# Kernel tuning notes

Hardware: AMD Instinct MI355X
Metric: run time of the kernel (lower is better)

## Reference

```python
import jax, jax.numpy as jnp
import numpy as np

B, T_MEL, T_TXT = 16, 2048, 1024
D_MODEL, D_ENC_M, D_ENC_T = 512, 512, 512
LN_EPS = 1e-5


def setup_inputs() -> dict:
    key = jax.random.key(0)
    ks = jax.random.split(key, 9)
    mel_encoding = jax.random.normal(ks[0], (B, T_MEL, D_ENC_M), dtype=jnp.float32)
    text_encoding = jax.random.normal(ks[1], (B, T_TXT, D_ENC_T), dtype=jnp.float32)
    mel_mask = jax.random.randint(ks[2], (B, T_MEL), 0, 2).astype(bool)
    mel_mask = mel_mask.at[:, 0].set(False)  # guarantee >=1 unmasked key per row
    src_mask = jax.random.randint(ks[3], (B, T_TXT), 0, 2).astype(bool)
    # Projection weights stored [in, out] (torch Linear does x @ W.T)
    sc = 1.0 / np.sqrt(D_ENC_M)
    Wq = jax.random.uniform(ks[4], (D_ENC_T, D_MODEL), jnp.float32, -sc, sc)
    Wk = jax.random.uniform(ks[5], (D_ENC_M, D_MODEL), jnp.float32, -sc, sc)
    Wv = jax.random.uniform(ks[6], (D_ENC_M, D_MODEL), jnp.float32, -sc, sc)
    ln_gamma = jnp.ones((D_MODEL,), jnp.float32)
    ln_beta = jnp.zeros((D_MODEL,), jnp.float32)
    return {"mel_encoding": mel_encoding, "text_encoding": text_encoding,
            "mel_mask": mel_mask, "src_mask": src_mask,
            "Wq": Wq, "Wk": Wk, "Wv": Wv,
            "ln_gamma": ln_gamma, "ln_beta": ln_beta}


def reference(mel_encoding, text_encoding, mel_mask, src_mask, Wq, Wk, Wv, ln_gamma, ln_beta):
    temperature = jnp.sqrt(jnp.float32(D_ENC_M))
    q = jnp.einsum('btd,dm->btm', text_encoding, Wq)   # [B, T_txt, d_model]
    k = jnp.einsum('bsd,dm->bsm', mel_encoding, Wk)    # [B, T_mel, d_model]
    v = jnp.einsum('bsd,dm->bsm', mel_encoding, Wv)
    # attn_mask = outer product of src_mask and mel_mask (True -> masked)
    attn_mask = src_mask[:, :, None] & mel_mask[:, None, :]  # [B, T_txt, T_mel]
    scores = jnp.einsum('btm,bsm->bts', q, k) / temperature
    scores = jnp.where(attn_mask, -jnp.inf, scores)
    attn = jax.nn.softmax(scores, axis=2)
    output = jnp.einsum('bts,bsm->btm', attn, v)
    # dropout is identity at inference; LayerNorm over last dim
    mean = jnp.mean(output, axis=-1, keepdims=True)
    var = jnp.var(output, axis=-1, keepdims=True)
    output = (output - mean) * jax.lax.rsqrt(var + LN_EPS) * ln_gamma + ln_beta
    return output, attn
```

## Files before the change

kernel.cpp:

```cpp
#include <hip/hip_runtime.h>

#define DEV __device__ __forceinline__

typedef __attribute__((ext_vector_type(8))) short short8v;
typedef __attribute__((ext_vector_type(4))) float f32x4;

DEV unsigned short f2bf(float f) {
  unsigned int x = __float_as_uint(f);
  x = x + 0x7FFFu + ((x >> 16) & 1u);
  return (unsigned short)(x >> 16);
}

DEV int swz_byte(int row, int kElem) {
  int chunk = ((kElem >> 3) ^ (row & 7));
  return row * 128 + (chunk << 4) + ((kElem & 7) << 1);
}

template <int ROUNDS>
DEV void stage(const unsigned short* __restrict__ g, int ld,
               unsigned short* tile, int tid) {
  const int wave = tid >> 6, l = tid & 63;
#pragma unroll
  for (int p = 0; p < ROUNDS; ++p) {
    const int r = (p << 5) + (wave << 3) + (l >> 3);
    const int c = ((l & 7) ^ (r & 7)) << 3;
    const unsigned short* src = g + (long)r * ld + c;
#if __has_builtin(__builtin_amdgcn_global_load_lds)
    unsigned short* dst = tile + (p << 11) + (wave << 9);
    __builtin_amdgcn_global_load_lds(
        (const __attribute__((address_space(1))) void*)src,
        (__attribute__((address_space(3))) void*)dst, 16, 0, 0);
#else
    short8v v = *reinterpret_cast<const short8v*>(src);
    *reinterpret_cast<short8v*>(reinterpret_cast<char*>(tile) +
                                (p << 12) + (wave << 10) + (l << 4)) = v;
#endif
  }
}

template <int BM, int EPI>
__global__ __launch_bounds__(256) void gemm_bf16(
    const unsigned short* __restrict__ A, const unsigned short* __restrict__ B,
    void* __restrict__ Cout, int M, int N, int K,
    long aBatch, long bBatch, long cBatch,
    const int* __restrict__ srcMask, const int* __restrict__ melMask,
    float scale, float* __restrict__ stats) {
  constexpr int NI = BM / 32;
  __shared__ unsigned short As[BM * 64];
  __shared__ unsigned short Bs[128 * 64];
  const int tid = threadIdx.x;
  const int lane = tid & 63;
  const int wave = tid >> 6;
  const int z = blockIdx.z;
  const unsigned short* Ab = A + (long)z * aBatch;
  const unsigned short* Bb = B + (long)z * bBatch;
  const long cOff = (long)z * cBatch;
  const int bm = blockIdx.y * BM;
  const int bn = blockIdx.x * 128;
  const int wr = (wave >> 1) * (BM / 2);
  const int wc = (wave & 1) * 64;
  const int l15 = lane & 15;
  const int lHi = lane >> 4;

  f32x4 acc[NI][4] = {};

  for (int kt = 0; kt < K; kt += 64) {
    stage<BM / 32>(Ab + (long)bm * K + kt, K, As, tid);
    stage<4>(Bb + (long)bn * K + kt, K, Bs, tid);
    __syncthreads();
#pragma unroll
    for (int ks = 0; ks < 2; ++ks) {
      const int k0 = (ks << 5) + (lHi << 3);
      short8v af[NI], bfr[4];
#pragma unroll
      for (int i = 0; i < NI; ++i)
        af[i] = *reinterpret_cast<const short8v*>(
            reinterpret_cast<const char*>(As) + swz_byte(wr + i * 16 + l15, k0));
#pragma unroll
      for (int j = 0; j < 4; ++j)
        bfr[j] = *reinterpret_cast<const short8v*>(
            reinterpret_cast<const char*>(Bs) + swz_byte(wc + j * 16 + l15, k0));
#pragma unroll
      for (int i = 0; i < NI; ++i)
#pragma unroll
        for (int j = 0; j < 4; ++j)
          acc[i][j] = __builtin_amdgcn_mfma_f32_16x16x32_bf16(af[i], bfr[j], acc[i][j], 0, 0, 0);
    }
    __syncthreads();
  }

  if constexpr (EPI >= 2) {
    __shared__ float redM[128][2];
    __shared__ float redS[128][2];
    const int wcIdx = wave & 1;
#pragma unroll
    for (int i = 0; i < NI; ++i) {
#pragma unroll
      for (int rr = 0; rr < 4; ++rr) {
        const int rloc = wr + i * 16 + lHi * 4 + rr;
        const int rb = bm + rloc;
        const bool sm = srcMask[z * 1024 + rb] != 0;
        float vals[4];
        float m_l = -3.0e38f;
#pragma unroll
        for (int j = 0; j < 4; ++j) {
          const int c = bn + wc + j * 16 + l15;
          const bool mm = melMask[z * 2048 + c] != 0;
          const float vf = (sm && mm) ? -1e30f : acc[i][j][rr] * scale;
          vals[j] = vf;
          if constexpr (EPI == 2)
            reinterpret_cast<unsigned short*>(Cout)[cOff + (long)rb * N + c] = f2bf(vf);
          else
            reinterpret_cast<float*>(Cout)[cOff + (long)rb * N + c] = vf;
          m_l = fmaxf(m_l, vf);
        }
        if (stats) {
#pragma unroll
          for (int o = 1; o < 16; o <<= 1) m_l = fmaxf(m_l, __shfl_xor(m_l, o, 64));
          float s_l = 0.f;
#pragma unroll
          for (int j = 0; j < 4; ++j) s_l += __expf(vals[j] - m_l);
#pragma unroll
          for (int o = 1; o < 16; o <<= 1) s_l += __shfl_xor(s_l, o, 64);
          if (l15 == 0) { redM[rloc][wcIdx] = m_l; redS[rloc][wcIdx] = s_l; }
        }
      }
    }
    if (stats) {
      __syncthreads();
      if (tid < 128) {
        const float m0 = redM[tid][0], m1 = redM[tid][1];
        const float Mx = fmaxf(m0, m1);
        const float S = redS[tid][0] * __expf(m0 - Mx) + redS[tid][1] * __expf(m1 - Mx);
        const long sidx = ((long)(z * 1024 + bm + tid)) * 32 + (long)blockIdx.x * 2;
        stats[sidx] = Mx;
        stats[sidx + 1] = S;
      }
    }
  } else {
#pragma unroll
    for (int i = 0; i < NI; ++i) {
#pragma unroll
      for (int j = 0; j < 4; ++j) {
        const int rb = bm + wr + i * 16 + lHi * 4;
        const int c = bn + wc + j * 16 + l15;
#pragma unroll
        for (int r = 0; r < 4; ++r) {
          const float v = acc[i][j][r];
          const long idx = cOff + (long)(rb + r) * N + c;
          if constexpr (EPI == 0)
            reinterpret_cast<unsigned short*>(Cout)[idx] = f2bf(v);
          else
            reinterpret_cast<float*>(Cout)[idx] = v;
        }
      }
    }
  }
}

__global__ __launch_bounds__(256) void softmax_finalize(
    unsigned short* __restrict__ sbf, const float* __restrict__ stats,
    float* __restrict__ attn) {
  const long row = blockIdx.x;
  const float* st = stats + row * 32;
  float Mx = -3.0e38f;
#pragma unroll
  for (int t = 0; t < 16; ++t) Mx = fmaxf(Mx, st[t * 2]);
  float S = 0.f;
#pragma unroll
  for (int t = 0; t < 16; ++t) S += st[t * 2 + 1] * __expf(st[t * 2] - Mx);
  const float inv = 1.0f / S;
  const int tid = threadIdx.x;
  unsigned short* sp = sbf + row * 2048 + tid * 8;
  float* ap = attn + row * 2048 + tid * 8;
  const short8v sv = *reinterpret_cast<const short8v*>(sp);
  float e[8];
#pragma unroll
  for (int u = 0; u < 8; ++u) {
    const float s = __uint_as_float(((unsigned)(unsigned short)sv[u]) << 16);
    e[u] = __expf(s - Mx) * inv;
  }
  float4 w0, w1;
  w0.x = e[0]; w0.y = e[1]; w0.z = e[2]; w0.w = e[3];
  w1.x = e[4]; w1.y = e[5]; w1.z = e[6]; w1.w = e[7];
  *reinterpret_cast<float4*>(ap) = w0;
  *reinterpret_cast<float4*>(ap + 4) = w1;
  short8v pk;
#pragma unroll
  for (int u = 0; u < 8; ++u) pk[u] = (short)f2bf(e[u]);
  *reinterpret_cast<short8v*>(sp) = pk;
}

__global__ __launch_bounds__(256) void softmax_rows(
    float* __restrict__ attn, unsigned short* __restrict__ pbf) {
  const long row = blockIdx.x;
  float4* p = reinterpret_cast<float4*>(attn + row * 2048);
  const int tid = threadIdx.x;
  float4 a = p[tid];
  float4 b = p[tid + 256];
  float m = fmaxf(fmaxf(fmaxf(a.x, a.y), fmaxf(a.z, a.w)),
                  fmaxf(fmaxf(b.x, b.y), fmaxf(b.z, b.w)));
#pragma unroll
  for (int o = 32; o; o >>= 1) m = fmaxf(m, __shfl_xor(m, o, 64));
  __shared__ float redm[4];
  if ((tid & 63) == 0) redm[tid >> 6] = m;
  __syncthreads();
  m = fmaxf(fmaxf(redm[0], redm[1]), fmaxf(redm[2], redm[3]));
  float e0 = __expf(a.x - m), e1 = __expf(a.y - m), e2 = __expf(a.z - m), e3 = __expf(a.w - m);
  float e4 = __expf(b.x - m), e5 = __expf(b.y - m), e6 = __expf(b.z - m), e7 = __expf(b.w - m);
  float s = ((e0 + e1) + (e2 + e3)) + ((e4 + e5) + (e6 + e7));
#pragma unroll
  for (int o = 32; o; o >>= 1) s += __shfl_xor(s, o, 64);
  __shared__ float reds[4];
  if ((tid & 63) == 0) reds[tid >> 6] = s;
  __syncthreads();
  s = (reds[0] + reds[1]) + (reds[2] + reds[3]);
  const float inv = 1.0f / s;
  a.x = e0 * inv; a.y = e1 * inv; a.z = e2 * inv; a.w = e3 * inv;
  b.x = e4 * inv; b.y = e5 * inv; b.z = e6 * inv; b.w = e7 * inv;
  p[tid] = a;
  p[tid + 256] = b;
  ushort4 o0, o1;
  o0.x = f2bf(a.x); o0.y = f2bf(a.y); o0.z = f2bf(a.z); o0.w = f2bf(a.w);
  o1.x = f2bf(b.x); o1.y = f2bf(b.y); o1.z = f2bf(b.z); o1.w = f2bf(b.w);
  *reinterpret_cast<ushort4*>(pbf + row * 2048 + tid * 4) = o0;
  *reinterpret_cast<ushort4*>(pbf + row * 2048 + 1024 + tid * 4) = o1;
}

__global__ __launch_bounds__(256) void f32_to_bf16(
    const float* __restrict__ in, unsigned short* __restrict__ out, long n) {
  long i = ((long)blockIdx.x * blockDim.x + threadIdx.x) * 8;
  const long stride = (long)gridDim.x * blockDim.x * 8;
  for (; i < n; i += stride) {
    const float4 a = *reinterpret_cast<const float4*>(in + i);
    const float4 b = *reinterpret_cast<const float4*>(in + i + 4);
    short8v o;
    o[0] = (short)f2bf(a.x); o[1] = (short)f2bf(a.y);
    o[2] = (short)f2bf(a.z); o[3] = (short)f2bf(a.w);
    o[4] = (short)f2bf(b.x); o[5] = (short)f2bf(b.y);
    o[6] = (short)f2bf(b.z); o[7] = (short)f2bf(b.w);
    *reinterpret_cast<short8v*>(out + i) = o;
  }
}

__global__ __launch_bounds__(256) void transpose_w3(
    const float* __restrict__ Wq, const float* __restrict__ Wk, const float* __restrict__ Wv,
    unsigned short* __restrict__ WqT, unsigned short* __restrict__ WkT,
    unsigned short* __restrict__ WvT) {
  __shared__ float t[32][33];
  const int zz = blockIdx.z;
  const float* W = zz == 0 ? Wq : zz == 1 ? Wk : Wv;
  unsigned short* WT = zz == 0 ? WqT : zz == 1 ? WkT : WvT;
  const int bx = blockIdx.x * 32;
  const int by = blockIdx.y * 32;
  const int tx = threadIdx.x, ty = threadIdx.y;
#pragma unroll
  for (int i = 0; i < 4; ++i)
    t[ty + i * 8][tx] = W[(long)(by + ty + i * 8) * 512 + bx + tx];
  __syncthreads();
#pragma unroll
  for (int i = 0; i < 4; ++i)
    WT[(long)(bx + ty + i * 8) * 512 + by + tx] = f2bf(t[tx][ty + i * 8]);
}

__global__ __launch_bounds__(64) void layernorm_rows(
    float* __restrict__ out, const float* __restrict__ gamma, const float* __restrict__ beta) {
  const long row = blockIdx.x;
  float4* p = reinterpret_cast<float4*>(out + row * 512);
  const int lane = threadIdx.x;
  float4 a = p[lane];
  float4 b = p[lane + 64];
  float s = ((a.x + a.y) + (a.z + a.w)) + ((b.x + b.y) + (b.z + b.w));
  float s2 = ((a.x * a.x + a.y * a.y) + (a.z * a.z + a.w * a.w)) +
             ((b.x * b.x + b.y * b.y) + (b.z * b.z + b.w * b.w));
#pragma unroll
  for (int o = 32; o; o >>= 1) {
    s += __shfl_xor(s, o, 64);
    s2 += __shfl_xor(s2, o, 64);
  }
  const float mean = s * (1.0f / 512.0f);
  const float var = s2 * (1.0f / 512.0f) - mean * mean;
  const float rstd = rsqrtf(var + 1e-5f);
  const float4 g0 = reinterpret_cast<const float4*>(gamma)[lane];
  const float4 g1 = reinterpret_cast<const float4*>(gamma)[lane + 64];
  const float4 c0 = reinterpret_cast<const float4*>(beta)[lane];
  const float4 c1 = reinterpret_cast<const float4*>(beta)[lane + 64];
  a.x = (a.x - mean) * rstd * g0.x + c0.x;
  a.y = (a.y - mean) * rstd * g0.y + c0.y;
  a.z = (a.z - mean) * rstd * g0.z + c0.z;
  a.w = (a.w - mean) * rstd * g0.w + c0.w;
  b.x = (b.x - mean) * rstd * g1.x + c1.x;
  b.y = (b.y - mean) * rstd * g1.y + c1.y;
  b.z = (b.z - mean) * rstd * g1.z + c1.z;
  b.w = (b.w - mean) * rstd * g1.w + c1.w;
  p[lane] = a;
  p[lane + 64] = b;
}

extern "C" void kernel_launch(void* const* d_in, const int* in_sizes, int n_in,
                              void* d_out, int out_size, void* d_ws, size_t ws_size,
                              hipStream_t stream) {
  const float* mel  = (const float*)d_in[0];
  const float* text = (const float*)d_in[1];
  const int* melMask = (const int*)d_in[2];
  const int* srcMask = (const int*)d_in[3];
  const float* Wq = (const float*)d_in[4];
  const float* Wk = (const float*)d_in[5];
  const float* Wv = (const float*)d_in[6];
  const float* gamma = (const float*)d_in[7];
  const float* beta  = (const float*)d_in[8];

  float* out = (float*)d_out;
  float* attn = (float*)d_out + (long)16 * 1024 * 512;

  unsigned short* ws = (unsigned short*)d_ws;
  unsigned short* wqT = ws;
  unsigned short* wkT = wqT + 512 * 512;
  unsigned short* wvT = wkT + 512 * 512;
  unsigned short* melbf  = wvT + 512 * 512;
  unsigned short* textbf = melbf + (long)16 * 2048 * 512;
  unsigned short* qbf = textbf + (long)16 * 1024 * 512;
  unsigned short* kbf = qbf + (long)16 * 1024 * 512;
  unsigned short* vT  = kbf + (long)16 * 2048 * 512;
  unsigned short* sbf = vT + (long)16 * 512 * 2048;
  float* stats = (float*)melbf;
  const bool bigws = ws_size >= 202899456ull;

  transpose_w3<<<dim3(16, 16, 3), dim3(32, 8), 0, stream>>>(Wq, Wk, Wv, wqT, wkT, wvT);
  f32_to_bf16<<<dim3(4096), 256, 0, stream>>>(mel, melbf, (long)16 * 2048 * 512);
  f32_to_bf16<<<dim3(2048), 256, 0, stream>>>(text, textbf, (long)16 * 1024 * 512);

  gemm_bf16<128, 0><<<dim3(4, 128, 1), 256, 0, stream>>>(
      textbf, wqT, qbf, 16384, 512, 512, 0, 0, 0, nullptr, nullptr, 1.0f, nullptr);
  gemm_bf16<128, 0><<<dim3(4, 256, 1), 256, 0, stream>>>(
      melbf, wkT, kbf, 32768, 512, 512, 0, 0, 0, nullptr, nullptr, 1.0f, nullptr);
  gemm_bf16<128, 0><<<dim3(16, 4, 16), 256, 0, stream>>>(
      wvT, melbf, vT, 512, 2048, 512, 0, (long)2048 * 512, (long)512 * 2048,
      nullptr, nullptr, 1.0f, nullptr);

  if (bigws) {
    gemm_bf16<128, 2><<<dim3(16, 8, 16), 256, 0, stream>>>(
        qbf, kbf, sbf, 1024, 2048, 512,
        (long)1024 * 512, (long)2048 * 512, (long)1024 * 2048,
        srcMask, melMask, 0.044194173824159216f, stats);
    softmax_finalize<<<dim3(16 * 1024), 256, 0, stream>>>(sbf, stats, attn);
    gemm_bf16<64, 1><<<dim3(4, 16, 16), 256, 0, stream>>>(
        sbf, vT, out, 1024, 512, 2048,
        (long)1024 * 2048, (long)512 * 2048, (long)1024 * 512,
        nullptr, nullptr, 1.0f, nullptr);
  } else {
    unsigned short* pbf = melbf;
    gemm_bf16<128, 3><<<dim3(16, 8, 16), 256, 0, stream>>>(
        qbf, kbf, attn, 1024, 2048, 512,
        (long)1024 * 512, (long)2048 * 512, (long)1024 * 2048,
        srcMask, melMask, 0.044194173824159216f, nullptr);
    softmax_rows<<<dim3(16 * 1024), 256, 0, stream>>>(attn, pbf);
    gemm_bf16<64, 1><<<dim3(4, 16, 16), 256, 0, stream>>>(
        pbf, vT, out, 1024, 512, 2048,
        (long)1024 * 2048, (long)512 * 2048, (long)1024 * 512,
        nullptr, nullptr, 1.0f, nullptr);
  }
  layernorm_rows<<<dim3(16 * 1024), 64, 0, stream>>>(out, gamma, beta);
}
```

Baseline: 312.7 us.

## Fuse K/V projections and softmax normalization into PV GEMM with XCD-aware block mapping

Merges the separate K and V projection GEMMs into one kernel that stages each mel tile once and computes both outputs. The softmax finalize pass is folded into the PV GEMM: it rebuilds the row max and sum from per-tile stats, normalizes scores on the fly while loading the A tile, and writes fp32 attn from only the first N-tile. Block indices are remapped so consecutive batches land on the same XCD group, aiming for better L2 reuse. The cost is extra exp work in the PV kernel, more LDS use in gemm_kv, and irregular attn writes from a subset of blocks.

Result: no change. 310.7 us (-0.7%).

```diff
diff --git a/kernel.cpp b/kernel.cpp
--- a/kernel.cpp
+++ b/kernel.cpp
@@ -9,6 +9,9 @@
   unsigned int x = __float_as_uint(f);
   x = x + 0x7FFFu + ((x >> 16) & 1u);
   return (unsigned short)(x >> 16);
+}
+DEV float bf2f(unsigned short u) {
+  return __uint_as_float(((unsigned)u) << 16);
 }
 
 DEV int swz_byte(int row, int kElem) {
@@ -38,7 +41,7 @@
   }
 }
 
-template <int BM, int EPI>
+template <int BM, int EPI, int GM>
 __global__ __launch_bounds__(256) void gemm_bf16(
     const unsigned short* __restrict__ A, const unsigned short* __restrict__ B,
     void* __restrict__ Cout, int M, int N, int K,
@@ -51,12 +54,23 @@
   const int tid = threadIdx.x;
   const int lane = tid & 63;
   const int wave = tid >> 6;
-  const int z = blockIdx.z;
+  int z, bmi, bni;
+  if constexpr (GM == 1) {
+    const int id = blockIdx.x;
+    z = (id & 7) | ((id >> 10) << 3);
+    const int ib = (id >> 3) & 127;
+    bni = ib & 15;
+    bmi = ib >> 4;
+  } else if constexpr (GM == 2) {
+    bmi = blockIdx.x; bni = blockIdx.y; z = blockIdx.z;
+  } else {
+    bni = blockIdx.x; bmi = blockIdx.y; z = blockIdx.z;
+  }
+  const int bm = bmi * BM;
+  const int bn = bni * 128;
   const unsigned short* Ab = A + (long)z * aBatch;
   const unsigned short* Bb = B + (long)z * bBatch;
   const long cOff = (long)z * cBatch;
-  const int bm = blockIdx.y * BM;
-  const int bn = blockIdx.x * 128;
   const int wr = (wave >> 1) * (BM / 2);
   const int wc = (wave & 1) * 64;
   const int l15 = lane & 15;
@@ -132,7 +146,7 @@
         const float m0 = redM[tid][0], m1 = redM[tid][1];
         const float Mx = fmaxf(m0, m1);
         const float S = redS[tid][0] * __expf(m0 - Mx) + redS[tid][1] * __expf(m1 - Mx);
-        const long sidx = ((long)(z * 1024 + bm + tid)) * 32 + (long)blockIdx.x * 2;
+        const long sidx = ((long)(z * 1024 + bm + tid)) * 32 + (long)bni * 2;
         stats[sidx] = Mx;
         stats[sidx + 1] = S;
       }
@@ -158,37 +172,176 @@
   }
 }
 
-__global__ __launch_bounds__(256) void softmax_finalize(
-    unsigned short* __restrict__ sbf, const float* __restrict__ stats,
-    float* __restrict__ attn) {
-  const long row = blockIdx.x;
-  const float* st = stats + row * 32;
-  float Mx = -3.0e38f;
-#pragma unroll
-  for (int t = 0; t < 16; ++t) Mx = fmaxf(Mx, st[t * 2]);
-  float S = 0.f;
-#pragma unroll
-  for (int t = 0; t < 16; ++t) S += st[t * 2 + 1] * __expf(st[t * 2] - Mx);
-  const float inv = 1.0f / S;
-  const int tid = threadIdx.x;
-  unsigned short* sp = sbf + row * 2048 + tid * 8;
-  float* ap = attn + row * 2048 + tid * 8;
-  const short8v sv = *reinterpret_cast<const short8v*>(sp);
-  float e[8];
-#pragma unroll
-  for (int u = 0; u < 8; ++u) {
-    const float s = __uint_as_float(((unsigned)(unsigned short)sv[u]) << 16);
-    e[u] = __expf(s - Mx) * inv;
-  }
-  float4 w0, w1;
-  w0.x = e[0]; w0.y = e[1]; w0.z = e[2]; w0.w = e[3];
-  w1.x = e[4]; w1.y = e[5]; w1.z = e[6]; w1.w = e[7];
-  *reinterpret_cast<float4*>(ap) = w0;
-  *reinterpret_cast<float4*>(ap + 4) = w1;
-  short8v pk;
-#pragma unroll
-  for (int u = 0; u < 8; ++u) pk[u] = (short)f2bf(e[u]);
-  *reinterpret_cast<short8v*>(sp) = pk;
+__global__ __launch_bounds__(256) void gemm_kv(
+    const unsigned short* __restrict__ mel, const unsigned short* __restrict__ WkT,
+    const unsigned short* __restrict__ WvT, unsigned short* __restrict__ kbf,
+    unsigned short* __restrict__ vT) {
+  __shared__ unsigned short Ms[128 * 64];
+  __shared__ unsigned short Ks[128 * 64];
+  __shared__ unsigned short Vs[128 * 64];
+  const int id = blockIdx.x;
+  const int z = (id & 7) | ((id >> 9) << 3);
+  const int ib = (id >> 3) & 63;
+  const int st = ib & 15, mt = ib >> 4;
+  const int bs = st * 128, bmm = mt * 128;
+  const int tid = threadIdx.x, lane = tid & 63, wave = tid >> 6;
+  const int wrS = (wave >> 1) * 64, wcM = (wave & 1) * 64;
+  const int l15 = lane & 15, lHi = lane >> 4;
+  const unsigned short* melB = mel + ((long)z * 2048 + bs) * 512;
+
+  f32x4 ak[4][4] = {};
+  f32x4 av[4][4] = {};
+
+  for (int kt = 0; kt < 512; kt += 64) {
+    stage<4>(melB + kt, 512, Ms, tid);
+    stage<4>(WkT + (long)bmm * 512 + kt, 512, Ks, tid);
+    stage<4>(WvT + (long)bmm * 512 + kt, 512, Vs, tid);
+    __syncthreads();
+#pragma unroll
+    for (int ks = 0; ks < 2; ++ks) {
+      const int k0 = (ks << 5) + (lHi << 3);
+      short8v mf[4], wf[4];
+#pragma unroll
+      for (int i = 0; i < 4; ++i)
+        mf[i] = *reinterpret_cast<const short8v*>(
+            reinterpret_cast<const char*>(Ms) + swz_byte(wrS + i * 16 + l15, k0));
+#pragma unroll
+      for (int j = 0; j < 4; ++j)
+        wf[j] = *reinterpret_cast<const short8v*>(
+            reinterpret_cast<const char*>(Ks) + swz_byte(wcM + j * 16 + l15, k0));
+#pragma unroll
+      for (int i = 0; i < 4; ++i)
+#pragma unroll
+        for (int j = 0; j < 4; ++j)
+          ak[i][j] = __builtin_amdgcn_mfma_f32_16x16x32_bf16(mf[i], wf[j], ak[i][j], 0, 0, 0);
+#pragma unroll
+      for (int j = 0; j < 4; ++j)
+        wf[j] = *reinterpret_cast<const short8v*>(
+            reinterpret_cast<const char*>(Vs) + swz_byte(wcM + j * 16 + l15, k0));
+#pragma unroll
+      for (int i = 0; i < 4; ++i)
+#pragma unroll
+        for (int j = 0; j < 4; ++j)
+          av[j][i] = __builtin_amdgcn_mfma_f32_16x16x32_bf16(wf[j], mf[i], av[j][i], 0, 0, 0);
+    }
+    __syncthreads();
+  }
+
+#pragma unroll
+  for (int i = 0; i < 4; ++i)
+#pragma unroll
+    for (int j = 0; j < 4; ++j) {
+      const int srow = bs + wrS + i * 16 + lHi * 4;
+      const int mcol = bmm + wcM + j * 16 + l15;
+      const int mrow = bmm + wcM + j * 16 + lHi * 4;
+      const int scol = bs + wrS + i * 16 + l15;
+#pragma unroll
+      for (int rr = 0; rr < 4; ++rr) {
+        kbf[((long)z * 2048 + srow + rr) * 512 + mcol] = f2bf(ak[i][j][rr]);
+        vT[((long)z * 512 + mrow + rr) * 2048 + scol] = f2bf(av[j][i][rr]);
+      }
+    }
+}
+
+__global__ __launch_bounds__(256) void pv_smx(
+    const unsigned short* __restrict__ sbf, const unsigned short* __restrict__ vT,
+    float* __restrict__ attn, float* __restrict__ out,
+    const float* __restrict__ stats) {
+  __shared__ unsigned short As[64 * 64];
+  __shared__ unsigned short Bs[128 * 64];
+  __shared__ float rowM[64], rowInv[64];
+  const int id = blockIdx.x;
+  const int z = (id & 7) | ((id >> 9) << 3);
+  const int ib = (id >> 3) & 63;
+  const int mt = ib & 15, nt = ib >> 4;
+  const int bm = mt * 64, bn = nt * 128;
+  const int tid = threadIdx.x, lane = tid & 63, wave = tid >> 6;
+  const bool writeAttn = (nt == 0);
+
+  if (tid < 64) {
+    const float* st = stats + ((long)(z * 1024 + bm + tid)) * 32;
+    float Mx = -3.0e38f;
+#pragma unroll
+    for (int t = 0; t < 16; ++t) Mx = fmaxf(Mx, st[t * 2]);
+    float S = 0.f;
+#pragma unroll
+    for (int t = 0; t < 16; ++t) S += st[t * 2 + 1] * __expf(st[t * 2] - Mx);
+    rowM[tid] = Mx;
+    rowInv[tid] = 1.0f / S;
+  }
+  __syncthreads();
+
+  const int ar = tid >> 2;
+  const int ac = (tid & 3) << 4;
+  const float mR = rowM[ar];
+  const float invR = rowInv[ar];
+  const long aOff = ((long)z * 1024 + bm + ar) * 2048 + ac;
+  const unsigned short* vTb = vT + ((long)z * 512 + bn) * 2048;
+  const int wr = (wave >> 1) * 32, wc = (wave & 1) * 64;
+  const int l15 = lane & 15, lHi = lane >> 4;
+
+  f32x4 acc[2][4] = {};
+
+  for (int kt = 0; kt < 2048; kt += 64) {
+    stage<4>(vTb + kt, 2048, Bs, tid);
+    const short8v s0 = *reinterpret_cast<const short8v*>(sbf + aOff + kt);
+    const short8v s1 = *reinterpret_cast<const short8v*>(sbf + aOff + kt + 8);
+    float e[16];
+#pragma unroll
+    for (int u = 0; u < 8; ++u) {
+      e[u] = __expf(bf2f((unsigned short)s0[u]) - mR) * invR;
+      e[u + 8] = __expf(bf2f((unsigned short)s1[u]) - mR) * invR;
+    }
+    if (writeAttn) {
+      float* ap = attn + aOff + kt;
+#pragma unroll
+      for (int g = 0; g < 4; ++g) {
+        float4 w;
+        w.x = e[g * 4]; w.y = e[g * 4 + 1]; w.z = e[g * 4 + 2]; w.w = e[g * 4 + 3];
+        *reinterpret_cast<float4*>(ap + g * 4) = w;
+      }
+    }
+    short8v pk0, pk1;
+#pragma unroll
+    for (int u = 0; u < 8; ++u) {
+      pk0[u] = (short)f2bf(e[u]);
+      pk1[u] = (short)f2bf(e[u + 8]);
+    }
+    *reinterpret_cast<short8v*>(reinterpret_cast<char*>(As) + swz_byte(ar, ac)) = pk0;
+    *reinterpret_cast<short8v*>(reinterpret_cast<char*>(As) + swz_byte(ar, ac + 8)) = pk1;
+    __syncthreads();
+
+#pragma unroll
+    for (int ks = 0; ks < 2; ++ks) {
+      const int k0 = (ks << 5) + (lHi << 3);
+      short8v af[2], bfr[4];
+#pragma unroll
+      for (int i = 0; i < 2; ++i)
+        af[i] = *reinterpret_cast<const short8v*>(
+            reinterpret_cast<const char*>(As) + swz_byte(wr + i * 16 + l15, k0));
+#pragma unroll
+      for (int j = 0; j < 4; ++j)
+        bfr[j] = *reinterpret_cast<const short8v*>(
+            reinterpret_cast<const char*>(Bs) + swz_byte(wc + j * 16 + l15, k0));
+#pragma unroll
+      for (int i = 0; i < 2; ++i)
+#pragma unroll
+        for (int j = 0; j < 4; ++j)
+          acc[i][j] = __builtin_amdgcn_mfma_f32_16x16x32_bf16(af[i], bfr[j], acc[i][j], 0, 0, 0);
+    }
+    __syncthreads();
+  }
+
+#pragma unroll
+  for (int i = 0; i < 2; ++i)
+#pragma unroll
+    for (int j = 0; j < 4; ++j) {
+      const int row = bm + wr + i * 16 + lHi * 4;
+      const int col = bn + wc + j * 16 + l15;
+#pragma unroll
+      for (int rr = 0; rr < 4; ++rr)
+        out[((long)z * 1024 + row + rr) * 512 + col] = acc[i][j][rr];
+    }
 }
 
 __global__ __launch_bounds__(256) void softmax_rows(
@@ -330,32 +483,24 @@
   f32_to_bf16<<<dim3(4096), 256, 0, stream>>>(mel, melbf, (long)16 * 2048 * 512);
   f32_to_bf16<<<dim3(2048), 256, 0, stream>>>(text, textbf, (long)16 * 1024 * 512);
 
-  gemm_bf16<128, 0><<<dim3(4, 128, 1), 256, 0, stream>>>(
+  gemm_bf16<128, 0, 2><<<dim3(128, 4, 1), 256, 0, stream>>>(
       textbf, wqT, qbf, 16384, 512, 512, 0, 0, 0, nullptr, nullptr, 1.0f, nullptr);
-  gemm_bf16<128, 0><<<dim3(4, 256, 1), 256, 0, stream>>>(
-      melbf, wkT, kbf, 32768, 512, 512, 0, 0, 0, nullptr, nullptr, 1.0f, nullptr);
-  gemm_bf16<128, 0><<<dim3(16, 4, 16), 256, 0, stream>>>(
-      wvT, melbf, vT, 512, 2048, 512, 0, (long)2048 * 512, (long)512 * 2048,
-      nullptr, nullptr, 1.0f, nullptr);
+  gemm_kv<<<dim3(1024), 256, 0, stream>>>(melbf, wkT, wvT, kbf, vT);
 
   if (bigws) {
-    gemm_bf16<128, 2><<<dim3(16, 8, 16), 256, 0, stream>>>(
+    gemm_bf16<128, 2, 1><<<dim3(2048), 256, 0, stream>>>(
         qbf, kbf, sbf, 1024, 2048, 512,
         (long)1024 * 512, (long)2048 * 512, (long)1024 * 2048,
         srcMask, melMask, 0.044194173824159216f, stats);
-    softmax_finalize<<<dim3(16 * 1024), 256, 0, stream>>>(sbf, stats, attn);
-    gemm_bf16<64, 1><<<dim3(4, 16, 16), 256, 0, stream>>>(
-        sbf, vT, out, 1024, 512, 2048,
-        (long)1024 * 2048, (long)512 * 2048, (long)1024 * 512,
-        nullptr, nullptr, 1.0f, nullptr);
+    pv_smx<<<dim3(1024), 256, 0, stream>>>(sbf, vT, attn, out, stats);
   } else {
     unsigned short* pbf = melbf;
-    gemm_bf16<128, 3><<<dim3(16, 8, 16), 256, 0, stream>>>(
+    gemm_bf16<128, 3, 0><<<dim3(16, 8, 16), 256, 0, stream>>>(
         qbf, kbf, attn, 1024, 2048, 512,
         (long)1024 * 512, (long)2048 * 512, (long)1024 * 2048,
         srcMask, melMask, 0.044194173824159216f, nullptr);
     softmax_rows<<<dim3(16 * 1024), 256, 0, stream>>>(attn, pbf);
-    gemm_bf16<64, 1><<<dim3(4, 16, 16), 256, 0, stream>>>(
+    gemm_bf16<64, 1, 0><<<dim3(4, 16, 16), 256, 0, stream>>>(
         pbf, vT, out, 1024, 512, 2048,
         (long)1024 * 2048, (long)512 * 2048, (long)1024 * 512,
         nullptr, nullptr, 1.0f, nullptr);
```
